# Optimization experiments

Measured on AMD Instinct MI355X. Metric: run time of the kernel, lower is better.

## Reference

```python
import jax, jax.numpy as jnp
import numpy as np

ALPHA = 0.5
SIGMA = 0.1
EPS = 1e-8
NUM_RISKS, B, T = 2, 8192, 64


def setup_inputs() -> dict:
    key = jax.random.key(0)
    k1, k2, k3, k4 = jax.random.split(key, 4)
    risk_outputs = jax.random.uniform(k1, (NUM_RISKS, B, T), dtype=jnp.float32)
    time_bins = jax.random.randint(k2, (B,), 0, T, dtype=jnp.int64)
    risk_indicators = jax.random.randint(k3, (B, NUM_RISKS), 0, 2).astype(bool)
    event_indicators = jax.random.randint(k4, (B,), 0, 2).astype(bool)
    return {
        "risk_outputs": risk_outputs,
        "time_bins": time_bins,
        "risk_indicators": risk_indicators,
        "event_indicators": event_indicators,
    }


def _deephit_loss(risk_outputs, time_bins, risk_indicators, event_indicators):
    ev = event_indicators  # (B,) bool: event occurred
    cens = ~ev             # (B,) bool: censored
    # pairwise mask M[i,j]: i censored, j had event, t_j <= t_i
    pair_mask = cens[:, None] & ev[None, :] & (time_bins[None, :] <= time_bins[:, None])

    def per_risk(pred, rind):
        # pred: (B, T), rind: (B,) bool
        # ---- likelihood: -mean(log p_i(t_i)) over samples with this risk's event
        probs = jnp.take_along_axis(pred, time_bins[:, None], axis=1)[:, 0]  # (B,)
        mask = rind & ev
        cnt = mask.sum()
        log_sum = jnp.where(mask, jnp.log(probs + EPS), 0.0).sum()
        ll = jnp.where(cnt > 0, -log_sum / jnp.maximum(cnt, 1).astype(pred.dtype), 0.0)
        # ---- ranking: sum sigmoid((F_i(t_i) - F_j(t_i)) / sigma) over valid (i,j) pairs
        cum = jnp.cumsum(pred, axis=1)          # (B, T)
        G = cum[:, time_bins].T                  # G[i, j] = cum[j, t_i]  -> (B, B)
        diff = jnp.diagonal(G)[:, None] - G      # cum[i,t_i] - cum[j,t_i]
        rl = jnp.where(pair_mask, jax.nn.sigmoid(diff / SIGMA), 0.0).sum()
        return ll, rl

    ll, rl = jax.vmap(per_risk)(risk_outputs, risk_indicators.T)
    return ALPHA * ll.sum() + (1.0 - ALPHA) * rl.sum()


def reference(risk_outputs, time_bins, risk_indicators, event_indicators):
    return _deephit_loss(risk_outputs, time_bins, risk_indicators, event_indicators)
```

## Files before the change

kernel.cpp:

```cpp
#include <hip/hip_runtime.h>
#include <math.h>


namespace {
constexpr int R  = 2;
constexpr int Bn = 8192;
constexpr int Tn = 64;
constexpr float INV_SIGMA = 10.0f;
constexpr float EPS       = 1e-8f;
}


__global__ void prep1(const int* __restrict__ tb, const int* __restrict__ ev,
                      int* limE, int* cbase, int* ncens, int* scatEw, int* scatCw) {
    __shared__ int hE[Tn], hC[Tn];
    int tid = threadIdx.x;
    if (tid < Tn) { hE[tid] = 0; hC[tid] = 0; }
    __syncthreads();
    for (int j = tid; j < Bn; j += 1024) {
        int t = tb[j];
        if (ev[j]) atomicAdd(&hE[t], 1);
        else       atomicAdd(&hC[t], 1);
    }
    __syncthreads();
    if (tid == 0) {
        int ae = 0, ac = 0;
        for (int t = 0; t < Tn; ++t) {
            scatEw[t] = ae; ae += hE[t]; limE[t] = ae;
            cbase[t] = ac; scatCw[t] = ac; ncens[t] = hC[t]; ac += hC[t];
        }
    }
}

__global__ void prep2(const int* __restrict__ tb, const int* __restrict__ ev,
                      int* scatEw, int* scatCw, int* pos) {
    int j = blockIdx.x * 256 + threadIdx.x;
    int t = tb[j];
    pos[j] = ev[j] ? atomicAdd(&scatEw[t], 1) : atomicAdd(&scatCw[t], 1);
}

__global__ void k_cum(const float* __restrict__ risk, const int* __restrict__ tb,
                      const int* __restrict__ rind, const int* __restrict__ ev,
                      const int* __restrict__ pos,
                      float* __restrict__ cumTs, float* __restrict__ aCens,
                      float* llsumArr, int* cntArr) {
    int w    = threadIdx.x >> 6;
    int lane = threadIdx.x & 63;
    int idx  = blockIdx.x * 4 + w;
    int i = idx & (Bn - 1);
    int r = idx >> 13;

    float v = risk[(size_t)idx * Tn + lane];
    float c = v;
#pragma unroll
    for (int o = 1; o < 64; o <<= 1) {
        float u = __shfl_up(c, o, 64);
        if (lane >= o) c += u;
    }

    int  ti = tb[i];
    bool e  = ev[i] != 0;
    int  po = pos[i];

    if (e)
        cumTs[((size_t)(r * Tn + lane)) * Bn + po] = c;

    float a = __shfl(c, ti, 64);
    float p = __shfl(v, ti, 64);
    if (lane == 0) {
        if (e) {
            if (rind[i * R + r]) {
                int slot = r * 32 + (blockIdx.x & 31);
                atomicAdd(&llsumArr[slot], logf(p + EPS));
                atomicAdd(&cntArr[slot], 1);
            }
        } else {
            aCens[r * Bn + po] = a;
        }
    }
}

__global__ void k_rank(const float* __restrict__ cumTs, const float* __restrict__ aCens,
                       const int* __restrict__ limE, const int* __restrict__ cbase,
                       const int* __restrict__ ncens, float* rlsumArr) {
    int t = blockIdx.z, r = blockIdx.y, ec = blockIdx.x;
    int ne = limE[t];
    if (ec * 1024 >= ne) return;
    int nc = ncens[t];
    if (nc == 0) return;

    int j0 = ec * 1024 + threadIdx.x * 4;
    const float* rowp = cumTs + ((size_t)(r * Tn + t)) * Bn;
    float4 c4 = *reinterpret_cast<const float4*>(rowp + j0);
    float c0 = (j0 + 0 < ne) ? c4.x * INV_SIGMA : INFINITY;
    float c1 = (j0 + 1 < ne) ? c4.y * INV_SIGMA : INFINITY;
    float c2 = (j0 + 2 < ne) ? c4.z * INV_SIGMA : INFINITY;
    float c3 = (j0 + 3 < ne) ? c4.w * INV_SIGMA : INFINITY;

    const float* aC = aCens + r * Bn + cbase[t];
    float s0 = 0.f, s1 = 0.f, s2 = 0.f, s3 = 0.f;
#pragma unroll 4
    for (int ii = 0; ii < nc; ++ii) {
        float a10 = aC[ii] * INV_SIGMA;
        s0 += __builtin_amdgcn_rcpf(1.f + __expf(c0 - a10));
        s1 += __builtin_amdgcn_rcpf(1.f + __expf(c1 - a10));
        s2 += __builtin_amdgcn_rcpf(1.f + __expf(c2 - a10));
        s3 += __builtin_amdgcn_rcpf(1.f + __expf(c3 - a10));
    }
    float s = (s0 + s1) + (s2 + s3);
#pragma unroll
    for (int o = 32; o > 0; o >>= 1) s += __shfl_down(s, o, 64);
    if ((threadIdx.x & 63) == 0) {
        int slot = r * 32 + ((blockIdx.z * 8 + blockIdx.x) & 31);
        atomicAdd(&rlsumArr[slot], s);
    }
}

__global__ void k_final(const float* llsumArr, const int* cntArr,
                        const float* rlsumArr, float* out) {
    int lane = threadIdx.x;
    float lg = llsumArr[lane];
    float rl = rlsumArr[lane];
    int   cn = cntArr[lane];
#pragma unroll
    for (int o = 1; o <= 16; o <<= 1) {
        lg += __shfl_xor(lg, o, 64);
        rl += __shfl_xor(rl, o, 64);
        cn += __shfl_xor(cn, o, 64);
    }
    float lg1 = __shfl(lg, 32, 64);
    float rl1 = __shfl(rl, 32, 64);
    int   cn1 = __shfl(cn, 32, 64);
    if (lane == 0) {
        float ll0 = (cn  > 0) ? (-lg  / (float)cn ) : 0.f;
        float ll1 = (cn1 > 0) ? (-lg1 / (float)cn1) : 0.f;
        out[0] = 0.5f * (ll0 + ll1) + 0.5f * (rl + rl1);
    }
}

extern "C" void kernel_launch(void* const* d_in, const int* in_sizes, int n_in,
                              void* d_out, int out_size, void* d_ws, size_t ws_size,
                              hipStream_t stream) {
    const float* risk = (const float*)d_in[0];
    const int* tb     = (const int*)d_in[1];
    const int* rind   = (const int*)d_in[2];
    const int* ev     = (const int*)d_in[3];

    char* ws = (char*)d_ws;
    float* llsumArr = (float*)(ws + 0);
    int*   cntArr   = (int*)(ws + 256);
    float* rlsumArr = (float*)(ws + 512);
    int*   limE     = (int*)(ws + 768);
    int*   cbase    = (int*)(ws + 1024);
    int*   ncens    = (int*)(ws + 1280);
    int*   scatEw   = (int*)(ws + 1536);
    int*   scatCw   = (int*)(ws + 1792);
    int*   pos      = (int*)(ws + 2048);
    float* aCens    = (float*)(ws + 34816);
    float* cumTs    = (float*)(ws + 100352);

    hipMemsetAsync(ws, 0, 768, stream);

    prep1<<<1, 1024, 0, stream>>>(tb, ev, limE, cbase, ncens, scatEw, scatCw);
    prep2<<<Bn / 256, 256, 0, stream>>>(tb, ev, scatEw, scatCw, pos);
    k_cum<<<(Bn * R) / 4, 256, 0, stream>>>(risk, tb, rind, ev, pos,
                                            cumTs, aCens, llsumArr, cntArr);
    dim3 gr(8, R, Tn);
    k_rank<<<gr, 256, 0, stream>>>(cumTs, aCens, limE, cbase, ncens, rlsumArr);
    k_final<<<1, 64, 0, stream>>>(llsumArr, cntArr, rlsumArr, (float*)d_out);
}
```

Before: 121.7 us.

## Merge prep kernels, gather by sorted index, and coalesce transposed cumsum writes

Merges the two preprocessing kernels and the memset into one block that builds per-time-bin sorted index lists for event and censored samples. The cumulative-sum kernel then walks those sorted lists, staging each 64x64 tile in shared memory so the transposed cumTs rows are written with coalesced stores instead of scattered ones. Censored samples compute only a masked reduction up to their bin rather than a full scan. This removes two launches and the uncoalesced scatter, at the cost of a larger single-block prep pass and gathered (non-sequential) row reads of the risk tensor.

```diff
diff --git a/kernel.cpp b/kernel.cpp
--- a/kernel.cpp
+++ b/kernel.cpp
@@ -11,11 +11,13 @@
 }
 
 
-__global__ void prep1(const int* __restrict__ tb, const int* __restrict__ ev,
-                      int* limE, int* cbase, int* ncens, int* scatEw, int* scatCw) {
-    __shared__ int hE[Tn], hC[Tn];
+__global__ void k_prep(const int* __restrict__ tb, const int* __restrict__ ev,
+                       int* limE, int* cbase, int* ncensG,
+                       int* esort, int* csort, int* accZero) {
+    __shared__ int hE[Tn], hC[Tn], wE[Tn], wC[Tn];
     int tid = threadIdx.x;
     if (tid < Tn) { hE[tid] = 0; hC[tid] = 0; }
+    if (tid < 192) accZero[tid] = 0;
     __syncthreads();
     for (int j = tid; j < Bn; j += 1024) {
         int t = tb[j];
@@ -26,56 +28,89 @@
     if (tid == 0) {
         int ae = 0, ac = 0;
         for (int t = 0; t < Tn; ++t) {
-            scatEw[t] = ae; ae += hE[t]; limE[t] = ae;
-            cbase[t] = ac; scatCw[t] = ac; ncens[t] = hC[t]; ac += hC[t];
-        }
-    }
-}
-
-__global__ void prep2(const int* __restrict__ tb, const int* __restrict__ ev,
-                      int* scatEw, int* scatCw, int* pos) {
-    int j = blockIdx.x * 256 + threadIdx.x;
-    int t = tb[j];
-    pos[j] = ev[j] ? atomicAdd(&scatEw[t], 1) : atomicAdd(&scatCw[t], 1);
-}
-
-__global__ void k_cum(const float* __restrict__ risk, const int* __restrict__ tb,
-                      const int* __restrict__ rind, const int* __restrict__ ev,
-                      const int* __restrict__ pos,
-                      float* __restrict__ cumTs, float* __restrict__ aCens,
-                      float* llsumArr, int* cntArr) {
-    int w    = threadIdx.x >> 6;
-    int lane = threadIdx.x & 63;
-    int idx  = blockIdx.x * 4 + w;
-    int i = idx & (Bn - 1);
-    int r = idx >> 13;
-
-    float v = risk[(size_t)idx * Tn + lane];
-    float c = v;
-#pragma unroll
-    for (int o = 1; o < 64; o <<= 1) {
-        float u = __shfl_up(c, o, 64);
-        if (lane >= o) c += u;
-    }
-
-    int  ti = tb[i];
-    bool e  = ev[i] != 0;
-    int  po = pos[i];
-
-    if (e)
-        cumTs[((size_t)(r * Tn + lane)) * Bn + po] = c;
-
-    float a = __shfl(c, ti, 64);
-    float p = __shfl(v, ti, 64);
-    if (lane == 0) {
-        if (e) {
-            if (rind[i * R + r]) {
-                int slot = r * 32 + (blockIdx.x & 31);
-                atomicAdd(&llsumArr[slot], logf(p + EPS));
-                atomicAdd(&cntArr[slot], 1);
+            wE[t] = ae; ae += hE[t]; limE[t] = ae;
+            wC[t] = ac; cbase[t] = ac; ncensG[t] = hC[t]; ac += hC[t];
+        }
+    }
+    __syncthreads();
+    for (int j = tid; j < Bn; j += 1024) {
+        int t = tb[j];
+        if (ev[j]) { int p = atomicAdd(&wE[t], 1); esort[p] = j; }
+        else       { int p = atomicAdd(&wC[t], 1); csort[p] = j; }
+    }
+}
+
+__global__ void __launch_bounds__(256)
+k_cum(const float* __restrict__ risk, const int* __restrict__ tb,
+      const int* __restrict__ rind,
+      const int* __restrict__ limE, const int* __restrict__ cbase,
+      const int* __restrict__ ncens,
+      const int* __restrict__ esort, const int* __restrict__ csort,
+      float* __restrict__ cumTs, float* __restrict__ aCens,
+      float* llsumArr, int* cntArr) {
+    const int r    = blockIdx.y;
+    const int lane = threadIdx.x & 63;
+    const int w    = threadIdx.x >> 6;
+    __shared__ float S[Tn][Tn + 1];
+    __shared__ int idxS[Tn];
+
+    if (blockIdx.x < 128) {
+        int nE = limE[Tn - 1];
+        int k0 = blockIdx.x * 64;
+        if (k0 >= nE) return;
+        int cnt = min(64, nE - k0);
+        if (threadIdx.x < cnt) idxS[threadIdx.x] = esort[k0 + threadIdx.x];
+        __syncthreads();
+        for (int s = 0; s < 16; ++s) {
+            int ls = w * 16 + s;
+            if (ls < cnt) {
+                int i = idxS[ls];
+                float v = risk[((size_t)r * Bn + i) * Tn + lane];
+                float c = v;
+#pragma unroll
+                for (int o = 1; o < 64; o <<= 1) {
+                    float u = __shfl_up(c, o, 64);
+                    if (lane >= o) c += u;
+                }
+                S[lane][ls] = c;
+                int ti = tb[i];
+                float p = __shfl(v, ti, 64);
+                if (lane == 0 && rind[i * R + r]) {
+                    int slot = r * 32 + ((k0 + ls) & 31);
+                    atomicAdd(&llsumArr[slot], logf(p + EPS));
+                    atomicAdd(&cntArr[slot], 1);
+                }
             }
-        } else {
-            aCens[r * Bn + po] = a;
+        }
+        __syncthreads();
+        float* dst = cumTs + ((size_t)r * Tn) * Bn + k0;
+        int col = threadIdx.x & 63;
+        int tr0 = threadIdx.x >> 6;
+        if (col < cnt) {
+#pragma unroll
+            for (int m = 0; m < 16; ++m) {
+                int t = m * 4 + tr0;
+                dst[(size_t)t * Bn + col] = S[t][col];
+            }
+        }
+    } else {
+        int nC = cbase[Tn - 1] + ncens[Tn - 1];
+        int k0 = (blockIdx.x - 128) * 64;
+        if (k0 >= nC) return;
+        int cnt = min(64, nC - k0);
+        if (threadIdx.x < cnt) idxS[threadIdx.x] = csort[k0 + threadIdx.x];
+        __syncthreads();
+        for (int s = 0; s < 16; ++s) {
+            int ls = w * 16 + s;
+            if (ls < cnt) {
+                int i  = idxS[ls];
+                int ti = tb[i];
+                float v = risk[((size_t)r * Bn + i) * Tn + lane];
+                v = (lane <= ti) ? v : 0.f;
+#pragma unroll
+                for (int o = 32; o > 0; o >>= 1) v += __shfl_down(v, o, 64);
+                if (lane == 0) aCens[r * Bn + k0 + ls] = v;
+            }
         }
     }
 }
@@ -153,18 +188,16 @@
     int*   limE     = (int*)(ws + 768);
     int*   cbase    = (int*)(ws + 1024);
     int*   ncens    = (int*)(ws + 1280);
-    int*   scatEw   = (int*)(ws + 1536);
-    int*   scatCw   = (int*)(ws + 1792);
-    int*   pos      = (int*)(ws + 2048);
-    float* aCens    = (float*)(ws + 34816);
-    float* cumTs    = (float*)(ws + 100352);
-
-    hipMemsetAsync(ws, 0, 768, stream);
-
-    prep1<<<1, 1024, 0, stream>>>(tb, ev, limE, cbase, ncens, scatEw, scatCw);
-    prep2<<<Bn / 256, 256, 0, stream>>>(tb, ev, scatEw, scatCw, pos);
-    k_cum<<<(Bn * R) / 4, 256, 0, stream>>>(risk, tb, rind, ev, pos,
-                                            cumTs, aCens, llsumArr, cntArr);
+    int*   esort    = (int*)(ws + 2048);
+    int*   csort    = (int*)(ws + 34816);
+    float* aCens    = (float*)(ws + 67584);
+    float* cumTs    = (float*)(ws + 133120);
+
+    k_prep<<<1, 1024, 0, stream>>>(tb, ev, limE, cbase, ncens, esort, csort,
+                                   (int*)ws);
+    dim3 gc(256, R);
+    k_cum<<<gc, 256, 0, stream>>>(risk, tb, rind, limE, cbase, ncens,
+                                  esort, csort, cumTs, aCens, llsumArr, cntArr);
     dim3 gr(8, R, Tn);
     k_rank<<<gr, 256, 0, stream>>>(cumTs, aCens, limE, cbase, ncens, rlsumArr);
     k_final<<<1, 64, 0, stream>>>(llsumArr, cntArr, rlsumArr, (float*)d_out);
```

Measured after the change: 116.8 us. 1.04x faster.
